# Kernel optimization log

Hardware: AMD Instinct MI355X
Metric: run time of the kernel (lower is better)

The kernel has to match this reference:

```python
import jax, jax.numpy as jnp
import numpy as np

HEADS = 8
EPS = 1e-5

def setup_inputs() -> dict:
    key = jax.random.key(0)
    ks = jax.random.split(key, 4)
    B, S, N, C = 1, 256, 384, 512
    msa = jax.random.normal(ks[0], (B, S, N, C), dtype=jnp.float32)
    mask = jnp.ones((B, S), dtype=jnp.int32)
    Wqkv = jax.random.normal(ks[1], (3 * C, C), dtype=jnp.float32) * (C ** -0.5)
    bqkv = jnp.zeros((3 * C,), dtype=jnp.float32)
    Wout = jax.random.normal(ks[2], (C, C), dtype=jnp.float32) * (C ** -0.5)
    bout = jnp.zeros((C,), dtype=jnp.float32)
    gamma = jnp.ones((C,), dtype=jnp.float32)
    beta = jnp.zeros((C,), dtype=jnp.float32)
    return {"msa": msa, "mask": mask, "Wqkv": Wqkv, "bqkv": bqkv,
            "Wout": Wout, "bout": bout, "gamma": gamma, "beta": beta}

def reference(msa, mask, Wqkv, bqkv, Wout, bout, gamma, beta):
    B, S, N, C = msa.shape
    H = HEADS
    Dh = C // H
    scale = Dh ** -0.5
    msa_t = jnp.transpose(msa, (0, 2, 1, 3))            # [B,N,S,C]
    qkv = msa_t @ Wqkv.T + bqkv                          # [B,N,S,3C]
    qkv = qkv.reshape(B, N, S, 3, H, Dh)
    q, k, v = qkv[..., 0, :, :], qkv[..., 1, :, :], qkv[..., 2, :, :]  # [B,N,S,H,Dh]
    attn = jnp.einsum('bnshc,bnthc->bhst', q, k) * scale  # reduce over N and head-dim
    attn = jnp.where(mask[:, None, None, :] == 0, -1e9, attn)
    attn = jax.nn.softmax(attn, axis=-1)                 # [B,H,S,S]
    out = jnp.einsum('bhst,bnthc->bnshc', attn, v).reshape(B, N, S, C)
    out = jnp.transpose(out, (0, 2, 1, 3))               # [B,S,N,C]
    out = out @ Wout.T + bout
    x = msa + out
    mu = jnp.mean(x, axis=-1, keepdims=True)
    var = jnp.mean((x - mu) ** 2, axis=-1, keepdims=True)
    return (x - mu) * jax.lax.rsqrt(var + EPS) * gamma + beta
```

## Files before the change

kernel.cpp:

```cpp
#include <hip/hip_runtime.h>

#define S_ 256
#define N_ 384
#define C_ 512
#define H_ 8
#define R_ (N_*S_)
#define SPLITK 16
#define NPK (N_/SPLITK)

typedef _Float16 f16;
typedef _Float16 f16x8 __attribute__((ext_vector_type(8)));
typedef _Float16 f16x4 __attribute__((ext_vector_type(4)));
typedef float f32x4 __attribute__((ext_vector_type(4)));

#define MFMA16(a,b,c) __builtin_amdgcn_mfma_f32_16x16x32_f16(a,b,c,0,0,0)

typedef __attribute__((address_space(3))) unsigned int as3_u32;
typedef __attribute__((address_space(1))) const unsigned int as1_u32;

__device__ __forceinline__ void gl_lds16(const void* g, void* l) {
    __builtin_amdgcn_global_load_lds((as1_u32*)(unsigned long long)g,
                                     (as3_u32*)(unsigned long long)l, 16, 0, 0);
}

__device__ __forceinline__ void stage_tile(const f16* __restrict__ Ab,
                                           const f16* __restrict__ Bb,
                                           int stride, f16* As_, f16* Bs_,
                                           int tid, int wid) {
#pragma unroll
    for (int i = 0; i < 2; ++i) {
        int id = (i << 8) + tid;
        int row = id >> 2;
        int g = (id & 3) ^ ((row >> 1) & 3);
        int lofs = ((i << 8) + (wid << 6)) << 4;
        gl_lds16(Ab + row * stride + (g << 3), (char*)As_ + lofs);
        gl_lds16(Bb + row * stride + (g << 3), (char*)Bs_ + lofs);
    }
}

__device__ __forceinline__ void frag_mma(const f16* As_, const f16* Bs_,
                                         int lane, int wr, int wc, f32x4 acc[4][4]) {
    int kg = lane >> 4;
    f16x8 af[4], bf[4];
#pragma unroll
    for (int m = 0; m < 4; ++m) {
        int row = wr + (m << 4) + (lane & 15);
        af[m] = *(const f16x8*)&As_[row * 32 + ((kg ^ ((row >> 1) & 3)) << 3)];
    }
#pragma unroll
    for (int j = 0; j < 4; ++j) {
        int row = wc + (j << 4) + (lane & 15);
        bf[j] = *(const f16x8*)&Bs_[row * 32 + ((kg ^ ((row >> 1) & 3)) << 3)];
    }
#pragma unroll
    for (int m = 0; m < 4; ++m)
#pragma unroll
        for (int j = 0; j < 4; ++j)
            acc[m][j] = MFMA16(af[m], bf[j], acc[m][j]);
}

__global__ __launch_bounds__(256) void k_prep(const float* __restrict__ Wqkv,
                                              const float* __restrict__ Wout,
                                              f16* __restrict__ Wq16, f16* __restrict__ Wo16) {
    int i = blockIdx.x * 256 + threadIdx.x;
    if (i < 1536 * C_) Wq16[i] = (f16)Wqkv[i];
    if (i < C_ * C_)   Wo16[i] = (f16)Wout[i];
}

__global__ __launch_bounds__(256) void k_cast(const float* __restrict__ msa,
                                              f16* __restrict__ msaT) {
    int t = blockIdx.x * 256 + threadIdx.x;
    int r = t >> 6, cg = t & 63;
    int n = r >> 8, s = r & 255;
    const float* src = msa + (s * N_ + n) * C_ + (cg << 3);
    float4 lo = *(const float4*)src;
    float4 hi = *(const float4*)(src + 4);
    f16x8 v;
    v[0]=(f16)lo.x; v[1]=(f16)lo.y; v[2]=(f16)lo.z; v[3]=(f16)lo.w;
    v[4]=(f16)hi.x; v[5]=(f16)hi.y; v[6]=(f16)hi.z; v[7]=(f16)hi.w;
    *(f16x8*)(msaT + r * C_ + (cg << 3)) = v;
}

__global__ __launch_bounds__(256) void k_qkv(const f16* __restrict__ msaT,
                                             const f16* __restrict__ W,
                                             const float* __restrict__ bqkv,
                                             f16* __restrict__ qk,
                                             f16* __restrict__ vT) {
    int wg = (blockIdx.x & 7) * 1152 + (blockIdx.x >> 3);
    int bx = wg / 12, by = wg % 12;
    int j0 = by << 7;
    int tid = threadIdx.x, lane = tid & 63, wid = tid >> 6;
    int wr = (wid >> 1) << 6, wc = (wid & 1) << 6;
    __shared__ f16 As[2][128 * 32];
    __shared__ f16 Bs[2][128 * 32];
    const f16* Abase = msaT + (bx << 7) * C_;
    const f16* Bbase = W + j0 * C_;
    f32x4 acc[4][4] = {};
    stage_tile(Abase, Bbase, C_, As[0], Bs[0], tid, wid);
    __syncthreads();
    for (int t = 0; t < 16; ++t) {
        int cur = t & 1;
        if (t < 15)
            stage_tile(Abase + ((t + 1) << 5), Bbase + ((t + 1) << 5), C_,
                       As[cur ^ 1], Bs[cur ^ 1], tid, wid);
        frag_mma(As[cur], Bs[cur], lane, wr, wc, acc);
        __syncthreads();
    }
#pragma unroll
    for (int m = 0; m < 4; ++m) {
        int rloc = wr + (m << 4) + ((lane >> 4) << 2);
        int r0 = (bx << 7) + rloc;
        if (by < 8) {
#pragma unroll
            for (int j = 0; j < 4; ++j) {
                int jc = j0 + wc + (j << 4) + (lane & 15);
                float bv = bqkv[jc];
#pragma unroll
                for (int q = 0; q < 4; ++q)
                    qk[(r0 + q) * 1024 + jc] = (f16)(acc[m][j][q] + bv);
            }
        } else {
            int n = bx >> 1, sBase = ((bx & 1) << 7) + rloc;
#pragma unroll
            for (int j = 0; j < 4; ++j) {
                int jl = (j0 - 1024) + wc + (j << 4) + (lane & 15);
                float bv = bqkv[1024 + jl];
                f16x4 vv;
#pragma unroll
                for (int q = 0; q < 4; ++q) vv[q] = (f16)(acc[m][j][q] + bv);
                *(f16x4*)(vT + ((n * H_ + (jl >> 6)) * 64 + (jl & 63)) * S_ + sBase) = vv;
            }
        }
    }
}

__global__ __launch_bounds__(256) void k_logits(const f16* __restrict__ qk,
                                                float* __restrict__ logP) {
    int wg = (blockIdx.x & 7) * 64 + (blockIdx.x >> 3);
    int sk = wg >> 5, rem = wg & 31, h = rem >> 2, sb = (rem >> 1) & 1, tb = rem & 1;
    int s0 = sb << 7, t0 = tb << 7, n0 = sk * NPK;
    int tid = threadIdx.x, lane = tid & 63, wid = tid >> 6;
    int wr = (wid >> 1) << 6, wc = (wid & 1) << 6;
    __shared__ f16 As[2][128 * 32];
    __shared__ f16 Bs[2][128 * 32];
    const f16* Aroot = qk + s0 * 1024 + (h << 6);
    const f16* Broot = qk + t0 * 1024 + 512 + (h << 6);
    f32x4 acc[4][4] = {};
    stage_tile(Aroot + n0 * S_ * 1024, Broot + n0 * S_ * 1024, 1024,
               As[0], Bs[0], tid, wid);
    __syncthreads();
    for (int t = 0; t < 2 * NPK; ++t) {
        int cur = t & 1;
        if (t < 2 * NPK - 1) {
            int tn = t + 1;
            int n = n0 + (tn >> 1), dh = (tn & 1) << 5;
            stage_tile(Aroot + n * S_ * 1024 + dh, Broot + n * S_ * 1024 + dh, 1024,
                       As[cur ^ 1], Bs[cur ^ 1], tid, wid);
        }
        frag_mma(As[cur], Bs[cur], lane, wr, wc, acc);
        __syncthreads();
    }
#pragma unroll
    for (int m = 0; m < 4; ++m) {
        int rloc = wr + (m << 4) + ((lane >> 4) << 2);
#pragma unroll
        for (int j = 0; j < 4; ++j) {
            int tc = t0 + wc + (j << 4) + (lane & 15);
#pragma unroll
            for (int q = 0; q < 4; ++q)
                logP[((sk * H_ + h) * S_ + s0 + rloc + q) * S_ + tc] = acc[m][j][q];
        }
    }
}

__global__ __launch_bounds__(256) void k_softmax(const float* __restrict__ logP,
                                                 const int* __restrict__ mask,
                                                 f16* __restrict__ attn) {
    int hs = blockIdx.x;
    int t = threadIdx.x, lane = t & 63, wid = t >> 6;
    float v = 0.f;
#pragma unroll
    for (int sk = 0; sk < SPLITK; ++sk)
        v += logP[(sk * H_ * S_ + hs) * S_ + t];
    v *= 0.125f;
    if (mask[t] == 0) v = -1e9f;
    __shared__ float redm[4], reds[4];
    float m_ = v;
    for (int o = 32; o > 0; o >>= 1) m_ = fmaxf(m_, __shfl_xor(m_, o));
    if (lane == 0) redm[wid] = m_;
    __syncthreads();
    float bm = fmaxf(fmaxf(redm[0], redm[1]), fmaxf(redm[2], redm[3]));
    float e = __expf(v - bm);
    float s_ = e;
    for (int o = 32; o > 0; o >>= 1) s_ += __shfl_xor(s_, o);
    if (lane == 0) reds[wid] = s_;
    __syncthreads();
    float tot = reds[0] + reds[1] + reds[2] + reds[3];
    attn[hs * S_ + t] = (f16)(e / tot);
}

__global__ __launch_bounds__(256) void k_pv(const f16* __restrict__ attn,
                                            const f16* __restrict__ vT,
                                            f16* __restrict__ attn_out) {
    int n = blockIdx.x >> 3, h = blockIdx.x & 7;
    int tid = threadIdx.x, lane = tid & 63, wid = tid >> 6;
    __shared__ f16 As[256 * 32];
    __shared__ f16 Bs[64 * 32];
    f32x4 acc[4][4] = {};
    for (int tt = 0; tt < 8; ++tt) {
        int t0 = tt << 5;
        __syncthreads();
#pragma unroll
        for (int i = 0; i < 4; ++i) {
            int id = tid + (i << 8);
            int sr = id >> 2, c4 = id & 3;
            *(f16x8*)&As[sr * 32 + (c4 << 3)] =
                *(const f16x8*)(attn + (h * S_ + sr) * S_ + t0 + (c4 << 3));
        }
        {
            int d = tid >> 2, c4 = tid & 3;
            *(f16x8*)&Bs[d * 32 + (c4 << 3)] =
                *(const f16x8*)(vT + ((n * H_ + h) * 64 + d) * S_ + t0 + (c4 << 3));
        }
        __syncthreads();
        f16x8 af[4], bf[4];
#pragma unroll
        for (int m = 0; m < 4; ++m)
            af[m] = *(const f16x8*)&As[(wid * 64 + m * 16 + (lane & 15)) * 32 + ((lane >> 4) << 3)];
#pragma unroll
        for (int j = 0; j < 4; ++j)
            bf[j] = *(const f16x8*)&Bs[(j * 16 + (lane & 15)) * 32 + ((lane >> 4) << 3)];
#pragma unroll
        for (int m = 0; m < 4; ++m)
#pragma unroll
            for (int j = 0; j < 4; ++j)
                acc[m][j] = MFMA16(af[m], bf[j], acc[m][j]);
    }
#pragma unroll
    for (int m = 0; m < 4; ++m) {
        int sl = wid * 64 + m * 16 + ((lane >> 4) << 2);
#pragma unroll
        for (int j = 0; j < 4; ++j) {
            int d = j * 16 + (lane & 15);
#pragma unroll
            for (int q = 0; q < 4; ++q)
                attn_out[(n * S_ + sl + q) * C_ + h * 64 + d] = (f16)acc[m][j][q];
        }
    }
}

__global__ __launch_bounds__(512) void k_out_ln(const f16* __restrict__ attn_out,
                                                const f16* __restrict__ Wo,
                                                const float* __restrict__ bout,
                                                const f16* __restrict__ msaT,
                                                const float* __restrict__ gamma,
                                                const float* __restrict__ beta,
                                                float* __restrict__ out) {
    int r0 = blockIdx.x << 6;
    int n = r0 >> 8, s0 = r0 & 255;
    int tid = threadIdx.x, lane = tid & 63, wid = tid >> 6;
    __shared__ f16 As[64 * 32];
    __shared__ f16 Bs[512 * 32];
    __shared__ float redS[8][64], redQ[8][64], muS[64], rsS[64];
    f32x4 acc[4][4] = {};
    for (int kt = 0; kt < 16; ++kt) {
        int c0 = kt << 5;
        __syncthreads();
        if (tid < 256) {
            int row = tid >> 2, c4 = tid & 3;
            *(f16x8*)&As[row * 32 + (c4 << 3)] =
                *(const f16x8*)(attn_out + (r0 + row) * C_ + c0 + (c4 << 3));
        }
#pragma unroll
        for (int i = 0; i < 4; ++i) {
            int id = tid + (i << 9);
            int row = id >> 2, c4 = id & 3;
            *(f16x8*)&Bs[row * 32 + (c4 << 3)] =
                *(const f16x8*)(Wo + row * C_ + c0 + (c4 << 3));
        }
        __syncthreads();
        f16x8 af[4], bf[4];
#pragma unroll
        for (int m = 0; m < 4; ++m)
            af[m] = *(const f16x8*)&As[((m << 4) + (lane & 15)) * 32 + ((lane >> 4) << 3)];
#pragma unroll
        for (int j = 0; j < 4; ++j)
            bf[j] = *(const f16x8*)&Bs[((wid << 6) + (j << 4) + (lane & 15)) * 32 + ((lane >> 4) << 3)];
#pragma unroll
        for (int m = 0; m < 4; ++m)
#pragma unroll
            for (int j = 0; j < 4; ++j)
                acc[m][j] = MFMA16(af[m], bf[j], acc[m][j]);
    }
    float psum[4][4] = {}, psq[4][4] = {};
#pragma unroll
    for (int m = 0; m < 4; ++m)
#pragma unroll
        for (int j = 0; j < 4; ++j) {
            int c = (wid << 6) + (j << 4) + (lane & 15);
            float bj = bout[c];
#pragma unroll
            for (int q = 0; q < 4; ++q) {
                int rl = (m << 4) + ((lane >> 4) << 2) + q;
                float x = acc[m][j][q] + bj + (float)msaT[(r0 + rl) * C_ + c];
                acc[m][j][q] = x;
                psum[m][q] += x;
                psq[m][q] += x * x;
            }
        }
#pragma unroll
    for (int m = 0; m < 4; ++m)
#pragma unroll
        for (int q = 0; q < 4; ++q)
            for (int o = 1; o < 16; o <<= 1) {
                psum[m][q] += __shfl_xor(psum[m][q], o);
                psq[m][q]  += __shfl_xor(psq[m][q], o);
            }
    if ((lane & 15) == 0) {
#pragma unroll
        for (int m = 0; m < 4; ++m)
#pragma unroll
            for (int q = 0; q < 4; ++q) {
                int rl = (m << 4) + ((lane >> 4) << 2) + q;
                redS[wid][rl] = psum[m][q];
                redQ[wid][rl] = psq[m][q];
            }
    }
    __syncthreads();
    if (tid < 64) {
        float t1 = 0.f, t2 = 0.f;
#pragma unroll
        for (int w = 0; w < 8; ++w) { t1 += redS[w][tid]; t2 += redQ[w][tid]; }
        float mu = t1 * (1.0f / 512.0f);
        float var = t2 * (1.0f / 512.0f) - mu * mu;
        muS[tid] = mu;
        rsS[tid] = rsqrtf(var + 1e-5f);
    }
    __syncthreads();
#pragma unroll
    for (int m = 0; m < 4; ++m)
#pragma unroll
        for (int j = 0; j < 4; ++j) {
            int c = (wid << 6) + (j << 4) + (lane & 15);
            float g = gamma[c], bb = beta[c];
#pragma unroll
            for (int q = 0; q < 4; ++q) {
                int rl = (m << 4) + ((lane >> 4) << 2) + q;
                int s = s0 + rl;
                float y = (acc[m][j][q] - muS[rl]) * rsS[rl] * g + bb;
                out[(s * N_ + n) * C_ + c] = y;
            }
        }
}

extern "C" void kernel_launch(void* const* d_in, const int* in_sizes, int n_in,
                              void* d_out, int out_size, void* d_ws, size_t ws_size,
                              hipStream_t stream) {
    const float* msa   = (const float*)d_in[0];
    const int*   mask  = (const int*)d_in[1];
    const float* Wqkv  = (const float*)d_in[2];
    const float* bqkv  = (const float*)d_in[3];
    const float* Wout  = (const float*)d_in[4];
    const float* bout  = (const float*)d_in[5];
    const float* gamma = (const float*)d_in[6];
    const float* beta  = (const float*)d_in[7];
    float* out = (float*)d_out;
    char* ws = (char*)d_ws;

    f16*   qk   = (f16*)(ws);
    f16*   vT   = (f16*)(ws + 201326592);
    f16*   msaT = (f16*)(ws + 301989888);
    float* logP = (float*)(ws + 402653184);
    f16*   attn = (f16*)(ws + 436207616);
    f16*   Wq16 = (f16*)(ws + 437256192);
    f16*   Wo16 = (f16*)(ws + 438829056);
    f16*   attn_out = qk;

    k_prep<<<dim3(3072), dim3(256), 0, stream>>>(Wqkv, Wout, Wq16, Wo16);
    k_cast<<<dim3(24576), dim3(256), 0, stream>>>(msa, msaT);
    k_qkv<<<dim3(9216), dim3(256), 0, stream>>>(msaT, Wq16, bqkv, qk, vT);
    k_logits<<<dim3(512), dim3(256), 0, stream>>>(qk, logP);
    k_softmax<<<dim3(2048), dim3(256), 0, stream>>>(logP, mask, attn);
    k_pv<<<dim3(3072), dim3(256), 0, stream>>>(attn, vT, attn_out);
    k_out_ln<<<dim3(1536), dim3(512), 0, stream>>>(attn_out, Wo16, bout, msaT, gamma, beta, out);
}
```

Baseline: 635.7 us.

## Stage QKV/PV epilogues through LDS, use async LDS loads in PV and out-proj

The QKV and PV epilogues now stage results in shared memory and write coalesced 16-byte rows instead of scattered 2-byte or 8-byte stores. The PV and output-projection GEMMs load tiles directly to LDS with a 64-wide K step and an XOR swizzle, replacing register round-trip copies. The logits split-K is doubled to 32 so more workgroups run. The partial logits now live in the output buffer, which frees workspace. In exchange there are extra barriers and LDS traffic, and the split-K change doubles the partial-logit data that softmax must reduce.

```diff
diff --git a/kernel.cpp b/kernel.cpp
--- a/kernel.cpp
+++ b/kernel.cpp
@@ -5,12 +5,11 @@
 #define C_ 512
 #define H_ 8
 #define R_ (N_*S_)
-#define SPLITK 16
+#define SPLITK 32
 #define NPK (N_/SPLITK)
 
 typedef _Float16 f16;
 typedef _Float16 f16x8 __attribute__((ext_vector_type(8)));
-typedef _Float16 f16x4 __attribute__((ext_vector_type(4)));
 typedef float f32x4 __attribute__((ext_vector_type(4)));
 
 #define MFMA16(a,b,c) __builtin_amdgcn_mfma_f32_16x16x32_f16(a,b,c,0,0,0)
@@ -23,10 +22,14 @@
                                      (as3_u32*)(unsigned long long)l, 16, 0, 0);
 }
 
-__device__ __forceinline__ void stage_tile(const f16* __restrict__ Ab,
-                                           const f16* __restrict__ Bb,
-                                           int stride, f16* As_, f16* Bs_,
-                                           int tid, int wid) {
+__device__ __forceinline__ int swz_off(int row, int g) {
+    return row*64 + (((g) ^ (row & 7)) << 3);
+}
+
+__device__ __forceinline__ void stage_tile32(const f16* __restrict__ Ab,
+                                             const f16* __restrict__ Bb,
+                                             int stride, f16* As_, f16* Bs_,
+                                             int tid, int wid) {
 #pragma unroll
     for (int i = 0; i < 2; ++i) {
         int id = (i << 8) + tid;
@@ -38,8 +41,8 @@
     }
 }
 
-__device__ __forceinline__ void frag_mma(const f16* As_, const f16* Bs_,
-                                         int lane, int wr, int wc, f32x4 acc[4][4]) {
+__device__ __forceinline__ void frag_mma32(const f16* As_, const f16* Bs_,
+                                           int lane, int wr, int wc, f32x4 acc[4][4]) {
     int kg = lane >> 4;
     f16x8 af[4], bf[4];
 #pragma unroll
@@ -57,6 +60,26 @@
 #pragma unroll
         for (int j = 0; j < 4; ++j)
             acc[m][j] = MFMA16(af[m], bf[j], acc[m][j]);
+}
+
+__device__ __forceinline__ void frag_mma64(const f16* As_, const f16* Bs_,
+                                           int lane, int wr, int wc, f32x4 acc[4][4]) {
+#pragma unroll
+    for (int ks = 0; ks < 64; ks += 32) {
+        int kg = (ks >> 3) + (lane >> 4);
+        f16x8 af[4], bf[4];
+#pragma unroll
+        for (int m = 0; m < 4; ++m)
+            af[m] = *(const f16x8*)&As_[swz_off(wr + (m << 4) + (lane & 15), kg)];
+#pragma unroll
+        for (int j = 0; j < 4; ++j)
+            bf[j] = *(const f16x8*)&Bs_[swz_off(wc + (j << 4) + (lane & 15), kg)];
+#pragma unroll
+        for (int m = 0; m < 4; ++m)
+#pragma unroll
+            for (int j = 0; j < 4; ++j)
+                acc[m][j] = MFMA16(af[m], bf[j], acc[m][j]);
+    }
 }
 
 __global__ __launch_bounds__(256) void k_prep(const float* __restrict__ Wqkv,
@@ -91,44 +114,76 @@
     int j0 = by << 7;
     int tid = threadIdx.x, lane = tid & 63, wid = tid >> 6;
     int wr = (wid >> 1) << 6, wc = (wid & 1) << 6;
-    __shared__ f16 As[2][128 * 32];
-    __shared__ f16 Bs[2][128 * 32];
+    __shared__ f16 SH[16384];
     const f16* Abase = msaT + (bx << 7) * C_;
     const f16* Bbase = W + j0 * C_;
     f32x4 acc[4][4] = {};
-    stage_tile(Abase, Bbase, C_, As[0], Bs[0], tid, wid);
+    stage_tile32(Abase, Bbase, C_, SH, SH + 8192, tid, wid);
     __syncthreads();
     for (int t = 0; t < 16; ++t) {
         int cur = t & 1;
         if (t < 15)
-            stage_tile(Abase + ((t + 1) << 5), Bbase + ((t + 1) << 5), C_,
-                       As[cur ^ 1], Bs[cur ^ 1], tid, wid);
-        frag_mma(As[cur], Bs[cur], lane, wr, wc, acc);
-        __syncthreads();
-    }
-#pragma unroll
-    for (int m = 0; m < 4; ++m) {
-        int rloc = wr + (m << 4) + ((lane >> 4) << 2);
-        int r0 = (bx << 7) + rloc;
-        if (by < 8) {
-#pragma unroll
-            for (int j = 0; j < 4; ++j) {
-                int jc = j0 + wc + (j << 4) + (lane & 15);
-                float bv = bqkv[jc];
-#pragma unroll
-                for (int q = 0; q < 4; ++q)
-                    qk[(r0 + q) * 1024 + jc] = (f16)(acc[m][j][q] + bv);
-            }
-        } else {
-            int n = bx >> 1, sBase = ((bx & 1) << 7) + rloc;
-#pragma unroll
-            for (int j = 0; j < 4; ++j) {
-                int jl = (j0 - 1024) + wc + (j << 4) + (lane & 15);
-                float bv = bqkv[1024 + jl];
-                f16x4 vv;
-#pragma unroll
-                for (int q = 0; q < 4; ++q) vv[q] = (f16)(acc[m][j][q] + bv);
-                *(f16x4*)(vT + ((n * H_ + (jl >> 6)) * 64 + (jl & 63)) * S_ + sBase) = vv;
+            stage_tile32(Abase + ((t + 1) << 5), Bbase + ((t + 1) << 5), C_,
+                         SH + ((cur ^ 1) << 12), SH + 8192 + ((cur ^ 1) << 12), tid, wid);
+        frag_mma32(SH + (cur << 12), SH + 8192 + (cur << 12), lane, wr, wc, acc);
+        __syncthreads();
+    }
+    if (by < 8) {
+#pragma unroll
+        for (int p = 0; p < 2; ++p) {
+            __syncthreads();
+#pragma unroll
+            for (int mm = 0; mm < 2; ++mm) {
+                int m = 2 * p + mm;
+                int rl = (m << 4) + ((lane >> 4) << 2);
+                int lrow = (wr >> 1) + rl - (p << 5);
+#pragma unroll
+                for (int j = 0; j < 4; ++j) {
+                    int col = wc + (j << 4) + (lane & 15);
+                    float bv = bqkv[j0 + col];
+#pragma unroll
+                    for (int q = 0; q < 4; ++q)
+                        SH[(lrow + q) * 136 + col] = (f16)(acc[m][j][q] + bv);
+                }
+            }
+            __syncthreads();
+#pragma unroll
+            for (int i = 0; i < 4; ++i) {
+                int u = tid + (i << 8);
+                int lrow = u >> 4, seg = u & 15;
+                int grow = (bx << 7) + ((lrow >> 5) << 6) + (p << 5) + (lrow & 31);
+                *(f16x8*)(qk + grow * 1024 + j0 + (seg << 3)) =
+                    *(const f16x8*)&SH[lrow * 136 + (seg << 3)];
+            }
+        }
+    } else {
+        int n = bx >> 1, t0g = (bx & 1) << 7;
+#pragma unroll
+        for (int p = 0; p < 2; ++p) {
+            __syncthreads();
+#pragma unroll
+            for (int m = 0; m < 4; ++m) {
+                int rl = wr + (m << 4) + ((lane >> 4) << 2);
+#pragma unroll
+                for (int jj = 0; jj < 2; ++jj) {
+                    int j = 2 * p + jj;
+                    int col = wc + (j << 4) + (lane & 15);
+                    int lcol = (col & 31) + ((col >> 6) << 5);
+                    float bv = bqkv[1024 + (by - 8) * 128 + col];
+#pragma unroll
+                    for (int q = 0; q < 4; ++q)
+                        SH[lcol * 136 + rl + q] = (f16)(acc[m][j][q] + bv);
+                }
+            }
+            __syncthreads();
+#pragma unroll
+            for (int i = 0; i < 4; ++i) {
+                int u = tid + (i << 8);
+                int lcol = u >> 4, seg = u & 15;
+                int col = (lcol & 31) + (p << 5) + ((lcol >> 5) << 6);
+                int jg = (by - 8) * 128 + col;
+                *(f16x8*)(vT + ((n * H_ + (jg >> 6)) * 64 + (jg & 63)) * S_ + t0g + (seg << 3)) =
+                    *(const f16x8*)&SH[lcol * 136 + (seg << 3)];
             }
         }
     }
@@ -136,28 +191,27 @@
 
 __global__ __launch_bounds__(256) void k_logits(const f16* __restrict__ qk,
                                                 float* __restrict__ logP) {
-    int wg = (blockIdx.x & 7) * 64 + (blockIdx.x >> 3);
+    int wg = (blockIdx.x & 7) * 128 + (blockIdx.x >> 3);
     int sk = wg >> 5, rem = wg & 31, h = rem >> 2, sb = (rem >> 1) & 1, tb = rem & 1;
     int s0 = sb << 7, t0 = tb << 7, n0 = sk * NPK;
     int tid = threadIdx.x, lane = tid & 63, wid = tid >> 6;
     int wr = (wid >> 1) << 6, wc = (wid & 1) << 6;
-    __shared__ f16 As[2][128 * 32];
-    __shared__ f16 Bs[2][128 * 32];
+    __shared__ f16 SH[16384];
     const f16* Aroot = qk + s0 * 1024 + (h << 6);
     const f16* Broot = qk + t0 * 1024 + 512 + (h << 6);
     f32x4 acc[4][4] = {};
-    stage_tile(Aroot + n0 * S_ * 1024, Broot + n0 * S_ * 1024, 1024,
-               As[0], Bs[0], tid, wid);
+    stage_tile32(Aroot + n0 * S_ * 1024, Broot + n0 * S_ * 1024, 1024,
+                 SH, SH + 8192, tid, wid);
     __syncthreads();
     for (int t = 0; t < 2 * NPK; ++t) {
         int cur = t & 1;
         if (t < 2 * NPK - 1) {
             int tn = t + 1;
             int n = n0 + (tn >> 1), dh = (tn & 1) << 5;
-            stage_tile(Aroot + n * S_ * 1024 + dh, Broot + n * S_ * 1024 + dh, 1024,
-                       As[cur ^ 1], Bs[cur ^ 1], tid, wid);
-        }
-        frag_mma(As[cur], Bs[cur], lane, wr, wc, acc);
+            stage_tile32(Aroot + n * S_ * 1024 + dh, Broot + n * S_ * 1024 + dh, 1024,
+                         SH + ((cur ^ 1) << 12), SH + 8192 + ((cur ^ 1) << 12), tid, wid);
+        }
+        frag_mma32(SH + (cur << 12), SH + 8192 + (cur << 12), lane, wr, wc, acc);
         __syncthreads();
     }
 #pragma unroll
@@ -204,47 +258,56 @@
                                             f16* __restrict__ attn_out) {
     int n = blockIdx.x >> 3, h = blockIdx.x & 7;
     int tid = threadIdx.x, lane = tid & 63, wid = tid >> 6;
-    __shared__ f16 As[256 * 32];
-    __shared__ f16 Bs[64 * 32];
+    __shared__ f16 SH[20480];
+    f16* As_ = SH;
+    f16* Bs_ = SH + 16384;
     f32x4 acc[4][4] = {};
-    for (int tt = 0; tt < 8; ++tt) {
-        int t0 = tt << 5;
+    const f16* Ab = attn + h * S_ * S_;
+    const f16* Bb = vT + (n * H_ + h) * 64 * S_;
+    for (int tt = 0; tt < 4; ++tt) {
+        int t0 = tt << 6;
+        __syncthreads();
+#pragma unroll
+        for (int i = 0; i < 8; ++i) {
+            int id = (i << 8) + tid;
+            int row = id >> 3, g = (id & 7) ^ (row & 7);
+            int lofs = ((i << 8) + (wid << 6)) << 4;
+            gl_lds16(Ab + row * S_ + t0 + (g << 3), (char*)As_ + lofs);
+        }
+#pragma unroll
+        for (int i = 0; i < 2; ++i) {
+            int id = (i << 8) + tid;
+            int row = id >> 3, g = (id & 7) ^ (row & 7);
+            int lofs = ((i << 8) + (wid << 6)) << 4;
+            gl_lds16(Bb + row * S_ + t0 + (g << 3), (char*)Bs_ + lofs);
+        }
+        __syncthreads();
+        frag_mma64(As_, Bs_, lane, wid << 6, 0, acc);
+    }
+#pragma unroll
+    for (int p = 0; p < 2; ++p) {
+        __syncthreads();
+#pragma unroll
+        for (int mm = 0; mm < 2; ++mm) {
+            int m = 2 * p + mm;
+            int rl = ((m & 1) << 4) + ((lane >> 4) << 2);
+            int lrow = (wid << 5) + rl;
+#pragma unroll
+            for (int j = 0; j < 4; ++j) {
+                int d = (j << 4) + (lane & 15);
+#pragma unroll
+                for (int q = 0; q < 4; ++q)
+                    SH[(lrow + q) * 72 + d] = (f16)acc[m][j][q];
+            }
+        }
         __syncthreads();
 #pragma unroll
         for (int i = 0; i < 4; ++i) {
-            int id = tid + (i << 8);
-            int sr = id >> 2, c4 = id & 3;
-            *(f16x8*)&As[sr * 32 + (c4 << 3)] =
-                *(const f16x8*)(attn + (h * S_ + sr) * S_ + t0 + (c4 << 3));
-        }
-        {
-            int d = tid >> 2, c4 = tid & 3;
-            *(f16x8*)&Bs[d * 32 + (c4 << 3)] =
-                *(const f16x8*)(vT + ((n * H_ + h) * 64 + d) * S_ + t0 + (c4 << 3));
-        }
-        __syncthreads();
-        f16x8 af[4], bf[4];
-#pragma unroll
-        for (int m = 0; m < 4; ++m)
-            af[m] = *(const f16x8*)&As[(wid * 64 + m * 16 + (lane & 15)) * 32 + ((lane >> 4) << 3)];
-#pragma unroll
-        for (int j = 0; j < 4; ++j)
-            bf[j] = *(const f16x8*)&Bs[(j * 16 + (lane & 15)) * 32 + ((lane >> 4) << 3)];
-#pragma unroll
-        for (int m = 0; m < 4; ++m)
-#pragma unroll
-            for (int j = 0; j < 4; ++j)
-                acc[m][j] = MFMA16(af[m], bf[j], acc[m][j]);
-    }
-#pragma unroll
-    for (int m = 0; m < 4; ++m) {
-        int sl = wid * 64 + m * 16 + ((lane >> 4) << 2);
-#pragma unroll
-        for (int j = 0; j < 4; ++j) {
-            int d = j * 16 + (lane & 15);
-#pragma unroll
-            for (int q = 0; q < 4; ++q)
-                attn_out[(n * S_ + sl + q) * C_ + h * 64 + d] = (f16)acc[m][j][q];
+            int u = tid + (i << 8);
+            int row = u >> 3, seg = u & 7;
+            int s = ((row >> 5) << 6) + (p << 5) + (row & 31);
+            *(f16x8*)(attn_out + (n * S_ + s) * C_ + (h << 6) + (seg << 3)) =
+                *(const f16x8*)&SH[row * 72 + (seg << 3)];
         }
     }
 }
@@ -259,38 +322,28 @@
     int r0 = blockIdx.x << 6;
     int n = r0 >> 8, s0 = r0 & 255;
     int tid = threadIdx.x, lane = tid & 63, wid = tid >> 6;
-    __shared__ f16 As[64 * 32];
-    __shared__ f16 Bs[512 * 32];
+    __shared__ f16 SH[36864];
+    f16* As_ = SH;
+    f16* Bs_ = SH + 4096;
     __shared__ float redS[8][64], redQ[8][64], muS[64], rsS[64];
     f32x4 acc[4][4] = {};
-    for (int kt = 0; kt < 16; ++kt) {
-        int c0 = kt << 5;
-        __syncthreads();
-        if (tid < 256) {
-            int row = tid >> 2, c4 = tid & 3;
-            *(f16x8*)&As[row * 32 + (c4 << 3)] =
-                *(const f16x8*)(attn_out + (r0 + row) * C_ + c0 + (c4 << 3));
-        }
-#pragma unroll
-        for (int i = 0; i < 4; ++i) {
-            int id = tid + (i << 9);
-            int row = id >> 2, c4 = id & 3;
-            *(f16x8*)&Bs[row * 32 + (c4 << 3)] =
-                *(const f16x8*)(Wo + row * C_ + c0 + (c4 << 3));
-        }
-        __syncthreads();
-        f16x8 af[4], bf[4];
-#pragma unroll
-        for (int m = 0; m < 4; ++m)
-            af[m] = *(const f16x8*)&As[((m << 4) + (lane & 15)) * 32 + ((lane >> 4) << 3)];
-#pragma unroll
-        for (int j = 0; j < 4; ++j)
-            bf[j] = *(const f16x8*)&Bs[((wid << 6) + (j << 4) + (lane & 15)) * 32 + ((lane >> 4) << 3)];
-#pragma unroll
-        for (int m = 0; m < 4; ++m)
-#pragma unroll
-            for (int j = 0; j < 4; ++j)
-                acc[m][j] = MFMA16(af[m], bf[j], acc[m][j]);
+    for (int kt = 0; kt < 8; ++kt) {
+        int c0 = kt << 6;
+        __syncthreads();
+        {
+            int row = tid >> 3, g = (tid & 7) ^ (row & 7);
+            int lofs = (wid << 6) << 4;
+            gl_lds16(attn_out + (r0 + row) * C_ + c0 + (g << 3), (char*)As_ + lofs);
+        }
+#pragma unroll
+        for (int i = 0; i < 8; ++i) {
+            int id = (i << 9) + tid;
+            int row = id >> 3, g = (id & 7) ^ (row & 7);
+            int lofs = ((i << 9) + (wid << 6)) << 4;
+            gl_lds16(Wo + row * C_ + c0 + (g << 3), (char*)Bs_ + lofs);
+        }
+        __syncthreads();
+        frag_mma64(As_, Bs_, lane, 0, wid << 6, acc);
     }
     float psum[4][4] = {}, psq[4][4] = {};
 #pragma unroll
@@ -370,16 +423,16 @@
     f16*   qk   = (f16*)(ws);
     f16*   vT   = (f16*)(ws + 201326592);
     f16*   msaT = (f16*)(ws + 301989888);
-    float* logP = (float*)(ws + 402653184);
-    f16*   attn = (f16*)(ws + 436207616);
-    f16*   Wq16 = (f16*)(ws + 437256192);
-    f16*   Wo16 = (f16*)(ws + 438829056);
+    f16*   attn = (f16*)(ws + 402653184);
+    f16*   Wq16 = (f16*)(ws + 403701760);
+    f16*   Wo16 = (f16*)(ws + 405274624);
+    float* logP = out;
     f16*   attn_out = qk;
 
     k_prep<<<dim3(3072), dim3(256), 0, stream>>>(Wqkv, Wout, Wq16, Wo16);
     k_cast<<<dim3(24576), dim3(256), 0, stream>>>(msa, msaT);
     k_qkv<<<dim3(9216), dim3(256), 0, stream>>>(msaT, Wq16, bqkv, qk, vT);
-    k_logits<<<dim3(512), dim3(256), 0, stream>>>(qk, logP);
+    k_logits<<<dim3(1024), dim3(256), 0, stream>>>(qk, logP);
     k_softmax<<<dim3(2048), dim3(256), 0, stream>>>(logP, mask, attn);
     k_pv<<<dim3(3072), dim3(256), 0, stream>>>(attn, vT, attn_out);
     k_out_ln<<<dim3(1536), dim3(512), 0, stream>>>(attn_out, Wo16, bout, msaT, gamma, beta, out);
```

Result: no change. 628.5 us (-1.1%).
